# Performance work log

Hardware: AMD Instinct MI355X
Metric: run time of the kernel (lower is better)

## Reference

```python
import jax, jax.numpy as jnp
import numpy as np

LOG_2PI = float(np.log(2.0 * np.pi))


def setup_inputs() -> dict:
    key = jax.random.key(0)
    k1, k2, k3, k4 = jax.random.split(key, 4)
    B, Tin, Tout, D = 32, 512, 2048, 256
    memory = jax.random.normal(k1, (B, Tin, D), dtype=jnp.float32)
    # durations in [1, 7) frames per token (mean ~4 -> ~Tout total frames)
    duration = jax.random.uniform(k2, (B, Tin), dtype=jnp.float32) * 6.0 + 1.0
    # positive Gaussian widths in [0.5, 2.0)
    sigma = jax.random.uniform(k3, (B, Tin), dtype=jnp.float32) * 1.5 + 0.5
    output_lengths = jnp.full((B,), Tout, dtype=jnp.int32)
    mask = jax.random.uniform(k4, (B, Tin)) < 0.1
    return {"memory": memory, "duration": duration, "sigma": sigma,
            "output_lengths": output_lengths, "mask": mask}


def reference(memory, duration, sigma, output_lengths, mask):
    # memory: (B,Tin,D); duration,sigma,mask: (B,Tin); output_lengths: (B,)
    Tout = int(np.max(np.asarray(output_lengths)))
    frames = jnp.arange(Tout, dtype=jnp.float32)[None, None, :]          # (1,1,Tout)
    center = jnp.cumsum(duration, axis=-1) - 0.5 * duration              # (B,Tin)
    c = center[..., None]                                                # (B,Tin,1)
    s = sigma[..., None]                                                 # (B,Tin,1)
    # Normal(loc=c, scale=s).log_prob(frames).exp()
    z = (frames - c) / s
    alignment = jnp.exp(-0.5 * z * z - jnp.log(s) - 0.5 * LOG_2PI)       # (B,Tin,Tout)
    alignment = jnp.where(mask[..., None], 0.0, alignment)               # masked_fill
    attn_weights = alignment / (jnp.sum(alignment, axis=1, keepdims=True) + 1e-8)
    # bmm(attn^T, memory): (B,Tout,Tin) @ (B,Tin,D) -> (B,Tout,D)
    upsampled = jnp.einsum('bit,bid->btd', attn_weights, memory)
    return upsampled, attn_weights
```

## Files before the change

### kernel.cpp

```cpp
#include <hip/hip_runtime.h>
#include <hip/hip_bf16.h>
#include <math.h>

#define HALF_LOG_2PI 0.9189385332046727f
#define WIN 32.0f
#define TILE_T 16

typedef float f32x4 __attribute__((ext_vector_type(4)));

__global__ void prep_k(const float* __restrict__ duration,
                       const float* __restrict__ sigma,
                       const void* __restrict__ mask,
                       float* __restrict__ center,
                       float* __restrict__ amp,
                       float* __restrict__ inv_sigma,
                       int B, int Tin) {
    __shared__ float s[1024];
    __shared__ int s_not[2];
    int b = blockIdx.x, i = threadIdx.x;
    if (i < 2) s_not[i] = 0;
    __syncthreads();
    {
        const unsigned int* mw = (const unsigned int*)mask;
        int nwords = (B * Tin) >> 2;
        int nI = 0, nF = 0;
        for (int k = i; k < nwords; k += blockDim.x) {
            unsigned int w = mw[k];
            nI |= (w != 0u && w != 1u);
            nF |= (w != 0u && w != 0x3F800000u);
        }
        if (nI) atomicOr(&s_not[0], 1);
        if (nF) atomicOr(&s_not[1], 1);
    }
    size_t gi = (size_t)b * Tin + i;
    float d = duration[gi];
    s[i] = d;
    __syncthreads();
    for (int off = 1; off < Tin; off <<= 1) {
        float v = (i >= off) ? s[i - off] : 0.0f;
        __syncthreads();
        s[i] += v;
        __syncthreads();
    }
    float c = s[i] - 0.5f * d;
    int mode = s_not[0] ? (s_not[1] ? 2 : 1) : 0;
    bool m;
    if (mode == 0)      m = ((const int*)mask)[gi] != 0;
    else if (mode == 1) m = ((const float*)mask)[gi] != 0.0f;
    else                m = ((const unsigned char*)mask)[gi] != 0;
    float sg = sigma[gi];
    center[gi]    = c;
    inv_sigma[gi] = 1.0f / sg;
    amp[gi]       = m ? 0.0f : __expf(-__logf(sg) - HALF_LOG_2PI);
}

__global__ __launch_bounds__(256) void denom_k(
        const float* __restrict__ center, const float* __restrict__ amp,
        const float* __restrict__ inv_sigma,
        float* __restrict__ inv_den, int* __restrict__ lo_out,
        int* __restrict__ cnt_out, int Tin, int Tout) {
    __shared__ float sc[1024], sa[1024], si[1024];
    int b = blockIdx.y;
    int t = blockIdx.x * 256 + threadIdx.x;
    for (int i = threadIdx.x; i < Tin; i += 256) {
        size_t g = (size_t)b * Tin + i;
        sc[i] = center[g]; sa[i] = amp[g]; si[i] = inv_sigma[g];
    }
    __syncthreads();
    if (t >= Tout) return;
    float tf = (float)t;
    int lo = 0, hi = Tin;
    while (lo < hi) {
        int mid = (lo + hi) >> 1;
        if (sc[mid] < tf - WIN) lo = mid + 1; else hi = mid;
    }
    float sum = 0.0f;
    int i = lo;
    for (; i < Tin; ++i) {
        float cc = sc[i];
        if (cc > tf + WIN) break;
        float z = (tf - cc) * si[i];
        sum += sa[i] * __expf(-0.5f * z * z);
    }
    size_t g = (size_t)b * Tout + t;
    inv_den[g]  = 1.0f / (sum + 1e-8f);
    lo_out[g]   = lo;
    cnt_out[g]  = i - lo;
}

__global__ __launch_bounds__(256) void attn_k(
        const float* __restrict__ center, const float* __restrict__ amp,
        const float* __restrict__ inv_sigma, const float* __restrict__ inv_den,
        float* __restrict__ attn, int Tin, int Tout) {
    int bi = blockIdx.x;
    int b  = bi / Tin;
    float c = center[bi], a = amp[bi], inv = inv_sigma[bi];
    const float* iden = inv_den + (size_t)b * Tout;
    float* row = attn + (size_t)bi * Tout;
    for (int t4 = threadIdx.x * 4; t4 < Tout; t4 += 256 * 4) {
        f32x4 rv;
        if ((float)(t4 + 3) < c - WIN || (float)t4 > c + WIN) {
            rv = (f32x4)0.0f;
        } else {
            #pragma unroll
            for (int j = 0; j < 4; ++j) {
                float dlt = (float)(t4 + j) - c;
                if (fabsf(dlt) < WIN) {
                    float z = dlt * inv;
                    rv[j] = a * __expf(-0.5f * z * z) * iden[t4 + j];
                } else rv[j] = 0.0f;
            }
        }
        __builtin_nontemporal_store(rv, (f32x4*)(row + t4));
    }
}

__global__ __launch_bounds__(256) void upsample_k(
        const float* __restrict__ mem, const float* __restrict__ center,
        const float* __restrict__ amp, const float* __restrict__ inv_sigma,
        const float* __restrict__ inv_den, const int* __restrict__ lo_ws,
        const int* __restrict__ cnt_ws, float* __restrict__ out,
        int Tin, int Tout, int D) {
    __shared__ __align__(16) float w_s[TILE_T][128];
    __shared__ float s_iden[TILE_T];
    __shared__ int s_lo, s_cnt;
    int nwg = gridDim.x;
    int wid = blockIdx.x;
    int work = wid;
    if ((nwg & 7) == 0) {
        int chunk = nwg >> 3;
        work = (wid & 7) * chunk + (wid >> 3);
    }
    int tpb = Tout / TILE_T;
    int b   = work / tpb;
    int t0  = (work - b * tpb) * TILE_T;
    int tid = threadIdx.x;
    if (tid == 0) {
        size_t g0 = (size_t)b * Tout + t0;
        size_t g1 = g0 + (TILE_T - 1);
        int lo0 = lo_ws[g0];
        int cnt = lo_ws[g1] + cnt_ws[g1] - lo0;
        s_lo  = lo0;
        s_cnt = cnt > 128 ? 128 : cnt;
    }
    if (tid < TILE_T) s_iden[tid] = inv_den[(size_t)b * Tout + t0 + tid];
    __syncthreads();
    int lo0 = s_lo, wcnt = s_cnt;
    #pragma unroll
    for (int rep = 0; rep < (TILE_T * 128) / 256; ++rep) {
        int id = tid + rep * 256;
        int f = id >> 7, w = id & 127;
        float wgt = 0.0f;
        int i = lo0 + w;
        if (w < wcnt && i < Tin) {
            size_t gi = (size_t)b * Tin + i;
            float dlt = (float)(t0 + f) - center[gi];
            if (fabsf(dlt) < WIN) {
                float z = dlt * inv_sigma[gi];
                wgt = amp[gi] * __expf(-0.5f * z * z) * s_iden[f];
            }
        }
        w_s[f][w] = wgt;
    }
    __syncthreads();
    for (int d = tid; d < D; d += 256) {
        float acc[TILE_T];
        #pragma unroll
        for (int f = 0; f < TILE_T; ++f) acc[f] = 0.0f;
        const float* mrow = mem + ((size_t)b * Tin + lo0) * D + d;
        int w4 = wcnt & ~3;
        for (int w = 0; w < w4; w += 4) {
            float m0 = mrow[(size_t)(w + 0) * D];
            float m1 = mrow[(size_t)(w + 1) * D];
            float m2 = mrow[(size_t)(w + 2) * D];
            float m3 = mrow[(size_t)(w + 3) * D];
            #pragma unroll
            for (int f = 0; f < TILE_T; ++f) {
                f32x4 wv = *(const f32x4*)&w_s[f][w];
                acc[f] += wv.x * m0 + wv.y * m1 + wv.z * m2 + wv.w * m3;
            }
        }
        for (int w = w4; w < wcnt; ++w) {
            float m0 = mrow[(size_t)w * D];
            #pragma unroll
            for (int f = 0; f < TILE_T; ++f) acc[f] += w_s[f][w] * m0;
        }
        float* orow = out + ((size_t)b * Tout + t0) * D + d;
        #pragma unroll
        for (int f = 0; f < TILE_T; ++f)
            __builtin_nontemporal_store(acc[f], orow + (size_t)f * D);
    }
}

extern "C" void kernel_launch(void* const* d_in, const int* in_sizes, int n_in,
                              void* d_out, int out_size, void* d_ws, size_t ws_size,
                              hipStream_t stream) {
    const float* memory   = (const float*)d_in[0];
    const float* duration = (const float*)d_in[1];
    const float* sigma    = (const float*)d_in[2];
    const void*  mask     = d_in[4];

    int B    = in_sizes[3];
    int Tin  = in_sizes[1] / B;
    int D    = in_sizes[0] / (B * Tin);
    int Tout = out_size / (B * (D + Tin));

    float* out_up   = (float*)d_out;
    float* out_attn = out_up + (size_t)B * Tout * D;

    float* center = (float*)d_ws;
    float* amp    = center + (size_t)B * Tin;
    float* inv    = amp    + (size_t)B * Tin;
    float* iden   = inv    + (size_t)B * Tin;
    int*   lo     = (int*)(iden + (size_t)B * Tout);
    int*   cnt    = lo + (size_t)B * Tout;

    prep_k<<<B, Tin, 0, stream>>>(duration, sigma, mask,
                                  center, amp, inv, B, Tin);
    denom_k<<<dim3((Tout + 255) / 256, B), 256, 0, stream>>>(
        center, amp, inv, iden, lo, cnt, Tin, Tout);
    attn_k<<<B * Tin, 256, 0, stream>>>(center, amp, inv, iden,
                                        out_attn, Tin, Tout);
    upsample_k<<<(B * Tout) / TILE_T, 256, 0, stream>>>(
        memory, center, amp, inv, iden, lo, cnt, out_up, Tin, Tout, D);
}
```

Before: 62.69 us.

## Fuse denominator, attention and upsample kernels into one interleaved launch

Removes the separate denominator kernel and merges attention-row writing and upsampling into a single launch whose blocks are interleaved two attention rows to one upsample tile. Each block stages center/amp/inv_sigma for its batch in shared memory and recomputes the normalising denominators locally: attention blocks compute them for the window of frames they cover, upsample blocks derive them from the weight tile they already built. This drops two launches and the workspace round-trip for inv_den/lo/cnt, and runs the write-bound attention output alongside the compute-bound upsample. In exchange, denominators are computed redundantly, the upsample tile shrinks to 8 frames so memory rows are reused less, and 12KB of shared memory per block may reduce occupancy.

Measured after the change: 76.51 us. +22.0%, slower.

```diff
diff --git a/kernel.cpp b/kernel.cpp
--- a/kernel.cpp
+++ b/kernel.cpp
@@ -4,7 +4,7 @@
 
 #define HALF_LOG_2PI 0.9189385332046727f
 #define WIN 32.0f
-#define TILE_T 16
+#define TILE_T 8
 
 typedef float f32x4 __attribute__((ext_vector_type(4)));
 
@@ -54,113 +54,119 @@
     amp[gi]       = m ? 0.0f : __expf(-__logf(sg) - HALF_LOG_2PI);
 }
 
-__global__ __launch_bounds__(256) void denom_k(
-        const float* __restrict__ center, const float* __restrict__ amp,
-        const float* __restrict__ inv_sigma,
-        float* __restrict__ inv_den, int* __restrict__ lo_out,
-        int* __restrict__ cnt_out, int Tin, int Tout) {
-    __shared__ float sc[1024], sa[1024], si[1024];
-    int b = blockIdx.y;
-    int t = blockIdx.x * 256 + threadIdx.x;
-    for (int i = threadIdx.x; i < Tin; i += 256) {
-        size_t g = (size_t)b * Tin + i;
-        sc[i] = center[g]; sa[i] = amp[g]; si[i] = inv_sigma[g];
-    }
-    __syncthreads();
-    if (t >= Tout) return;
-    float tf = (float)t;
-    int lo = 0, hi = Tin;
-    while (lo < hi) {
-        int mid = (lo + hi) >> 1;
-        if (sc[mid] < tf - WIN) lo = mid + 1; else hi = mid;
-    }
-    float sum = 0.0f;
-    int i = lo;
-    for (; i < Tin; ++i) {
-        float cc = sc[i];
-        if (cc > tf + WIN) break;
-        float z = (tf - cc) * si[i];
-        sum += sa[i] * __expf(-0.5f * z * z);
-    }
-    size_t g = (size_t)b * Tout + t;
-    inv_den[g]  = 1.0f / (sum + 1e-8f);
-    lo_out[g]   = lo;
-    cnt_out[g]  = i - lo;
-}
-
-__global__ __launch_bounds__(256) void attn_k(
-        const float* __restrict__ center, const float* __restrict__ amp,
-        const float* __restrict__ inv_sigma, const float* __restrict__ inv_den,
-        float* __restrict__ attn, int Tin, int Tout) {
-    int bi = blockIdx.x;
-    int b  = bi / Tin;
-    float c = center[bi], a = amp[bi], inv = inv_sigma[bi];
-    const float* iden = inv_den + (size_t)b * Tout;
-    float* row = attn + (size_t)bi * Tout;
-    for (int t4 = threadIdx.x * 4; t4 < Tout; t4 += 256 * 4) {
-        f32x4 rv;
-        if ((float)(t4 + 3) < c - WIN || (float)t4 > c + WIN) {
-            rv = (f32x4)0.0f;
-        } else {
-            #pragma unroll
-            for (int j = 0; j < 4; ++j) {
-                float dlt = (float)(t4 + j) - c;
-                if (fabsf(dlt) < WIN) {
-                    float z = dlt * inv;
-                    rv[j] = a * __expf(-0.5f * z * z) * iden[t4 + j];
-                } else rv[j] = 0.0f;
-            }
-        }
-        __builtin_nontemporal_store(rv, (f32x4*)(row + t4));
-    }
-}
-
-__global__ __launch_bounds__(256) void upsample_k(
+__global__ __launch_bounds__(256) void fused_k(
         const float* __restrict__ mem, const float* __restrict__ center,
         const float* __restrict__ amp, const float* __restrict__ inv_sigma,
-        const float* __restrict__ inv_den, const int* __restrict__ lo_ws,
-        const int* __restrict__ cnt_ws, float* __restrict__ out,
-        int Tin, int Tout, int D) {
+        float* __restrict__ attn, float* __restrict__ out,
+        int nAttn, int nUp, int Tin, int Tout, int D) {
+    __shared__ __align__(16) float sc[1024], sa[1024], si[1024];
     __shared__ __align__(16) float w_s[TILE_T][128];
-    __shared__ float s_iden[TILE_T];
-    __shared__ int s_lo, s_cnt;
-    int nwg = gridDim.x;
+    __shared__ float s_iden[80];
+
+    int nwg = nAttn + nUp;
     int wid = blockIdx.x;
     int work = wid;
     if ((nwg & 7) == 0) {
         int chunk = nwg >> 3;
         work = (wid & 7) * chunk + (wid >> 3);
     }
+    int aid = -1, uid = -1;
+    if (nAttn == 2 * nUp) {
+        int q = work / 3, r = work - q * 3;
+        if (r == 2) uid = q; else aid = q * 2 + r;
+    } else {
+        if (work < nAttn) aid = work; else uid = work - nAttn;
+    }
+
+    int tid = threadIdx.x;
     int tpb = Tout / TILE_T;
-    int b   = work / tpb;
-    int t0  = (work - b * tpb) * TILE_T;
-    int tid = threadIdx.x;
-    if (tid == 0) {
-        size_t g0 = (size_t)b * Tout + t0;
-        size_t g1 = g0 + (TILE_T - 1);
-        int lo0 = lo_ws[g0];
-        int cnt = lo_ws[g1] + cnt_ws[g1] - lo0;
-        s_lo  = lo0;
-        s_cnt = cnt > 128 ? 128 : cnt;
-    }
-    if (tid < TILE_T) s_iden[tid] = inv_den[(size_t)b * Tout + t0 + tid];
-    __syncthreads();
-    int lo0 = s_lo, wcnt = s_cnt;
+    int b = (aid >= 0) ? (aid / Tin) : (uid / tpb);
+
+    for (int i = tid; i < Tin; i += 256) {
+        size_t g = (size_t)b * Tin + i;
+        sc[i] = center[g]; sa[i] = amp[g]; si[i] = inv_sigma[g];
+    }
+    __syncthreads();
+
+    if (aid >= 0) {
+        int i = aid - b * Tin;
+        float c = sc[i], a = sa[i], inv = si[i];
+        int tlo = max(0, (int)ceilf(c - WIN));
+        int thi = min(Tout - 1, (int)floorf(c + WIN));
+        int nf  = thi - tlo + 1;
+        if (tid < nf) {
+            float tf = (float)(tlo + tid);
+            int lo = 0, hi = Tin;
+            while (lo < hi) {
+                int mid = (lo + hi) >> 1;
+                if (sc[mid] < tf - WIN) lo = mid + 1; else hi = mid;
+            }
+            float sum = 0.0f;
+            for (int j = lo; j < Tin; ++j) {
+                float cc = sc[j];
+                if (cc > tf + WIN) break;
+                float z = (tf - cc) * si[j];
+                sum += sa[j] * __expf(-0.5f * z * z);
+            }
+            s_iden[tid] = 1.0f / (sum + 1e-8f);
+        }
+        __syncthreads();
+        float* row = attn + (size_t)aid * Tout;
+        for (int t4 = tid * 4; t4 < Tout; t4 += 256 * 4) {
+            f32x4 rv;
+            if (t4 + 3 < tlo || t4 > thi) {
+                rv = (f32x4)0.0f;
+            } else {
+                #pragma unroll
+                for (int j = 0; j < 4; ++j) {
+                    int t = t4 + j;
+                    if (t >= tlo && t <= thi) {
+                        float z = ((float)t - c) * inv;
+                        rv[j] = a * __expf(-0.5f * z * z) * s_iden[t - tlo];
+                    } else rv[j] = 0.0f;
+                }
+            }
+            __builtin_nontemporal_store(rv, (f32x4*)(row + t4));
+        }
+        return;
+    }
+
+    int t0 = (uid - b * tpb) * TILE_T;
+    float tfl = (float)t0 - WIN;
+    float tfh = (float)(t0 + TILE_T - 1) + WIN;
+    int lo0 = 0;
+    {   int hi = Tin;
+        while (lo0 < hi) { int mid = (lo0 + hi) >> 1;
+                           if (sc[mid] < tfl) lo0 = mid + 1; else hi = mid; } }
+    int hi1 = lo0;
+    {   int hh = Tin;
+        while (hi1 < hh) { int mid = (hi1 + hh) >> 1;
+                           if (sc[mid] <= tfh) hi1 = mid + 1; else hh = mid; } }
+    int wcnt = hi1 - lo0;
+    if (wcnt > 128) wcnt = 128;
     #pragma unroll
     for (int rep = 0; rep < (TILE_T * 128) / 256; ++rep) {
         int id = tid + rep * 256;
         int f = id >> 7, w = id & 127;
         float wgt = 0.0f;
         int i = lo0 + w;
-        if (w < wcnt && i < Tin) {
-            size_t gi = (size_t)b * Tin + i;
-            float dlt = (float)(t0 + f) - center[gi];
+        if (w < wcnt) {
+            float dlt = (float)(t0 + f) - sc[i];
             if (fabsf(dlt) < WIN) {
-                float z = dlt * inv_sigma[gi];
-                wgt = amp[gi] * __expf(-0.5f * z * z) * s_iden[f];
+                float z = dlt * si[i];
+                wgt = sa[i] * __expf(-0.5f * z * z);
             }
         }
         w_s[f][w] = wgt;
+    }
+    __syncthreads();
+    {
+        int f = tid >> 5, lane = tid & 31;
+        float p = w_s[f][lane] + w_s[f][lane + 32]
+                + w_s[f][lane + 64] + w_s[f][lane + 96];
+        #pragma unroll
+        for (int m = 16; m >= 1; m >>= 1) p += __shfl_xor(p, m, 64);
+        if (lane == 0) s_iden[f] = 1.0f / (p + 1e-8f);
     }
     __syncthreads();
     for (int d = tid; d < D; d += 256) {
@@ -188,7 +194,8 @@
         float* orow = out + ((size_t)b * Tout + t0) * D + d;
         #pragma unroll
         for (int f = 0; f < TILE_T; ++f)
-            __builtin_nontemporal_store(acc[f], orow + (size_t)f * D);
+            __builtin_nontemporal_store(acc[f] * s_iden[f],
+                                        orow + (size_t)f * D);
     }
 }
 
@@ -211,16 +218,12 @@
     float* center = (float*)d_ws;
     float* amp    = center + (size_t)B * Tin;
     float* inv    = amp    + (size_t)B * Tin;
-    float* iden   = inv    + (size_t)B * Tin;
-    int*   lo     = (int*)(iden + (size_t)B * Tout);
-    int*   cnt    = lo + (size_t)B * Tout;
 
     prep_k<<<B, Tin, 0, stream>>>(duration, sigma, mask,
                                   center, amp, inv, B, Tin);
-    denom_k<<<dim3((Tout + 255) / 256, B), 256, 0, stream>>>(
-        center, amp, inv, iden, lo, cnt, Tin, Tout);
-    attn_k<<<B * Tin, 256, 0, stream>>>(center, amp, inv, iden,
-                                        out_attn, Tin, Tout);
-    upsample_k<<<(B * Tout) / TILE_T, 256, 0, stream>>>(
-        memory, center, amp, inv, iden, lo, cnt, out_up, Tin, Tout, D);
+    int nAttn = B * Tin;
+    int nUp   = (B * Tout) / TILE_T;
+    fused_k<<<nAttn + nUp, 256, 0, stream>>>(
+        memory, center, amp, inv, out_attn, out_up,
+        nAttn, nUp, Tin, Tout, D);
 }
```

## Merge attention-write and upsample kernels into one interleaved launch

Applied to the files above, without the earlier changes.

Replaces the separate attention-row writer and upsample kernels with one kernel whose blocks alternate between the two roles by the parity of the work index. Each attention block now writes four rows instead of one. The aim is to overlap the bandwidth-heavy attention stores with the upsample compute and memory reads, and to save one kernel launch. The role mapping assumes equal counts of attention and upsample blocks (B*Tin/4 == B*Tout/16). That holds here, but with other shapes some work would be dropped or indices would run past the end.

Result: no change. 63.81 us (+1.8%).

```diff
diff --git a/kernel.cpp b/kernel.cpp
--- a/kernel.cpp
+++ b/kernel.cpp
@@ -88,39 +88,12 @@
     cnt_out[g]  = i - lo;
 }
 
-__global__ __launch_bounds__(256) void attn_k(
-        const float* __restrict__ center, const float* __restrict__ amp,
-        const float* __restrict__ inv_sigma, const float* __restrict__ inv_den,
-        float* __restrict__ attn, int Tin, int Tout) {
-    int bi = blockIdx.x;
-    int b  = bi / Tin;
-    float c = center[bi], a = amp[bi], inv = inv_sigma[bi];
-    const float* iden = inv_den + (size_t)b * Tout;
-    float* row = attn + (size_t)bi * Tout;
-    for (int t4 = threadIdx.x * 4; t4 < Tout; t4 += 256 * 4) {
-        f32x4 rv;
-        if ((float)(t4 + 3) < c - WIN || (float)t4 > c + WIN) {
-            rv = (f32x4)0.0f;
-        } else {
-            #pragma unroll
-            for (int j = 0; j < 4; ++j) {
-                float dlt = (float)(t4 + j) - c;
-                if (fabsf(dlt) < WIN) {
-                    float z = dlt * inv;
-                    rv[j] = a * __expf(-0.5f * z * z) * iden[t4 + j];
-                } else rv[j] = 0.0f;
-            }
-        }
-        __builtin_nontemporal_store(rv, (f32x4*)(row + t4));
-    }
-}
-
-__global__ __launch_bounds__(256) void upsample_k(
+__global__ __launch_bounds__(256) void attn_up_k(
         const float* __restrict__ mem, const float* __restrict__ center,
         const float* __restrict__ amp, const float* __restrict__ inv_sigma,
         const float* __restrict__ inv_den, const int* __restrict__ lo_ws,
-        const int* __restrict__ cnt_ws, float* __restrict__ out,
-        int Tin, int Tout, int D) {
+        const int* __restrict__ cnt_ws, float* __restrict__ attn,
+        float* __restrict__ out, int Tin, int Tout, int D) {
     __shared__ __align__(16) float w_s[TILE_T][128];
     __shared__ float s_iden[TILE_T];
     __shared__ int s_lo, s_cnt;
@@ -131,10 +104,42 @@
         int chunk = nwg >> 3;
         work = (wid & 7) * chunk + (wid >> 3);
     }
+    int r = work & 1, q = work >> 1;
+    int tid = threadIdx.x;
+
+    if (r == 0) {
+        int rpb = Tin >> 2;
+        int b   = q / rpb;
+        int i0  = (q - b * rpb) * 4;
+        const float* iden = inv_den + (size_t)b * Tout;
+        #pragma unroll
+        for (int rr = 0; rr < 4; ++rr) {
+            int bi = b * Tin + i0 + rr;
+            float c = center[bi], a = amp[bi], inv = inv_sigma[bi];
+            float* row = attn + (size_t)bi * Tout;
+            for (int t4 = tid * 4; t4 < Tout; t4 += 256 * 4) {
+                f32x4 rv;
+                if ((float)(t4 + 3) < c - WIN || (float)t4 > c + WIN) {
+                    rv = (f32x4)0.0f;
+                } else {
+                    #pragma unroll
+                    for (int j = 0; j < 4; ++j) {
+                        float dlt = (float)(t4 + j) - c;
+                        if (fabsf(dlt) < WIN) {
+                            float z = dlt * inv;
+                            rv[j] = a * __expf(-0.5f * z * z) * iden[t4 + j];
+                        } else rv[j] = 0.0f;
+                    }
+                }
+                __builtin_nontemporal_store(rv, (f32x4*)(row + t4));
+            }
+        }
+        return;
+    }
+
     int tpb = Tout / TILE_T;
-    int b   = work / tpb;
-    int t0  = (work - b * tpb) * TILE_T;
-    int tid = threadIdx.x;
+    int b   = q / tpb;
+    int t0  = (q - b * tpb) * TILE_T;
     if (tid == 0) {
         size_t g0 = (size_t)b * Tout + t0;
         size_t g1 = g0 + (TILE_T - 1);
@@ -219,8 +224,9 @@
                                   center, amp, inv, B, Tin);
     denom_k<<<dim3((Tout + 255) / 256, B), 256, 0, stream>>>(
         center, amp, inv, iden, lo, cnt, Tin, Tout);
-    attn_k<<<B * Tin, 256, 0, stream>>>(center, amp, inv, iden,
-                                        out_attn, Tin, Tout);
-    upsample_k<<<(B * Tout) / TILE_T, 256, 0, stream>>>(
-        memory, center, amp, inv, iden, lo, cnt, out_up, Tin, Tout, D);
-}
+    int nAttnQ = (B * Tin) / 4;
+    int nUp    = (B * Tout) / TILE_T;
+    attn_up_k<<<nAttnQ + nUp, 256, 0, stream>>>(
+        memory, center, amp, inv, iden, lo, cnt,
+        out_attn, out_up, Tin, Tout, D);
+}
```

## Fuse prep into denominator kernel and batch four attention rows per block

Applied to the files above, without the earlier changes.

The separate prep kernel is merged into the denominator kernel. Each block recomputes the per-batch cumulative sum with a per-thread chunk plus wavefront shuffle scan, and only the first block in x writes center/amp/inv_sigma to global memory. This removes one kernel launch and the global round-trip for those arrays. The attention kernel now handles four rows per block, cutting the grid size by four to reduce block scheduling overhead. In exchange, the prefix scan and mask-format scan are repeated in every denom block, and the scan assumes Tin is a multiple of 256 and at most 2048.

Result: slower. 65.35 us (+4.2%).

```diff
diff --git a/kernel.cpp b/kernel.cpp
--- a/kernel.cpp
+++ b/kernel.cpp
@@ -8,23 +8,24 @@
 
 typedef float f32x4 __attribute__((ext_vector_type(4)));
 
-__global__ void prep_k(const float* __restrict__ duration,
-                       const float* __restrict__ sigma,
-                       const void* __restrict__ mask,
-                       float* __restrict__ center,
-                       float* __restrict__ amp,
-                       float* __restrict__ inv_sigma,
-                       int B, int Tin) {
-    __shared__ float s[1024];
+__global__ __launch_bounds__(256) void denom_prep_k(
+        const float* __restrict__ duration, const float* __restrict__ sigma,
+        const void* __restrict__ mask,
+        float* __restrict__ center, float* __restrict__ amp,
+        float* __restrict__ inv_sigma, float* __restrict__ inv_den,
+        int* __restrict__ lo_out, int* __restrict__ cnt_out,
+        int B, int Tin, int Tout) {
+    __shared__ float sc[1024], sa[1024], si[1024];
+    __shared__ float s_wsum[4];
     __shared__ int s_not[2];
-    int b = blockIdx.x, i = threadIdx.x;
-    if (i < 2) s_not[i] = 0;
+    int b = blockIdx.y, tid = threadIdx.x;
+    if (tid < 2) s_not[tid] = 0;
     __syncthreads();
     {
         const unsigned int* mw = (const unsigned int*)mask;
         int nwords = (B * Tin) >> 2;
         int nI = 0, nF = 0;
-        for (int k = i; k < nwords; k += blockDim.x) {
+        for (int k = tid; k < nwords; k += 256) {
             unsigned int w = mw[k];
             nI |= (w != 0u && w != 1u);
             nF |= (w != 0u && w != 0x3F800000u);
@@ -32,41 +33,42 @@
         if (nI) atomicOr(&s_not[0], 1);
         if (nF) atomicOr(&s_not[1], 1);
     }
-    size_t gi = (size_t)b * Tin + i;
-    float d = duration[gi];
-    s[i] = d;
-    __syncthreads();
-    for (int off = 1; off < Tin; off <<= 1) {
-        float v = (i >= off) ? s[i - off] : 0.0f;
-        __syncthreads();
-        s[i] += v;
-        __syncthreads();
-    }
-    float c = s[i] - 0.5f * d;
+    int E = Tin >> 8;
+    int base = tid * E;
+    float x[8];
+    float tsum = 0.0f;
+    const float* drow = duration + (size_t)b * Tin;
+    for (int e = 0; e < E; ++e) { x[e] = drow[base + e]; tsum += x[e]; }
+    float isc = tsum;
+    int lane = tid & 63, wv = tid >> 6;
+    #pragma unroll
+    for (int d = 1; d < 64; d <<= 1) {
+        float v = __shfl_up(isc, d, 64);
+        if (lane >= d) isc += v;
+    }
+    if (lane == 63) s_wsum[wv] = isc;
+    __syncthreads();
+    float excl = isc - tsum;
+    for (int w2 = 0; w2 < wv; ++w2) excl += s_wsum[w2];
     int mode = s_not[0] ? (s_not[1] ? 2 : 1) : 0;
-    bool m;
-    if (mode == 0)      m = ((const int*)mask)[gi] != 0;
-    else if (mode == 1) m = ((const float*)mask)[gi] != 0.0f;
-    else                m = ((const unsigned char*)mask)[gi] != 0;
-    float sg = sigma[gi];
-    center[gi]    = c;
-    inv_sigma[gi] = 1.0f / sg;
-    amp[gi]       = m ? 0.0f : __expf(-__logf(sg) - HALF_LOG_2PI);
-}
-
-__global__ __launch_bounds__(256) void denom_k(
-        const float* __restrict__ center, const float* __restrict__ amp,
-        const float* __restrict__ inv_sigma,
-        float* __restrict__ inv_den, int* __restrict__ lo_out,
-        int* __restrict__ cnt_out, int Tin, int Tout) {
-    __shared__ float sc[1024], sa[1024], si[1024];
-    int b = blockIdx.y;
-    int t = blockIdx.x * 256 + threadIdx.x;
-    for (int i = threadIdx.x; i < Tin; i += 256) {
-        size_t g = (size_t)b * Tin + i;
-        sc[i] = center[g]; sa[i] = amp[g]; si[i] = inv_sigma[g];
-    }
-    __syncthreads();
+    float run = excl;
+    for (int e = 0; e < E; ++e) {
+        float c = run + 0.5f * x[e];
+        run += x[e];
+        int i = base + e;
+        size_t gi = (size_t)b * Tin + i;
+        bool m;
+        if (mode == 0)      m = ((const int*)mask)[gi] != 0;
+        else if (mode == 1) m = ((const float*)mask)[gi] != 0.0f;
+        else                m = ((const unsigned char*)mask)[gi] != 0;
+        float sg = sigma[gi];
+        float a  = m ? 0.0f : __expf(-__logf(sg) - HALF_LOG_2PI);
+        float is = 1.0f / sg;
+        sc[i] = c; sa[i] = a; si[i] = is;
+        if (blockIdx.x == 0) { center[gi] = c; amp[gi] = a; inv_sigma[gi] = is; }
+    }
+    __syncthreads();
+    int t = blockIdx.x * 256 + tid;
     if (t >= Tout) return;
     float tf = (float)t;
     int lo = 0, hi = Tin;
@@ -83,35 +85,42 @@
         sum += sa[i] * __expf(-0.5f * z * z);
     }
     size_t g = (size_t)b * Tout + t;
-    inv_den[g]  = 1.0f / (sum + 1e-8f);
-    lo_out[g]   = lo;
-    cnt_out[g]  = i - lo;
+    inv_den[g] = 1.0f / (sum + 1e-8f);
+    lo_out[g]  = lo;
+    cnt_out[g] = i - lo;
 }
 
 __global__ __launch_bounds__(256) void attn_k(
         const float* __restrict__ center, const float* __restrict__ amp,
         const float* __restrict__ inv_sigma, const float* __restrict__ inv_den,
         float* __restrict__ attn, int Tin, int Tout) {
-    int bi = blockIdx.x;
-    int b  = bi / Tin;
-    float c = center[bi], a = amp[bi], inv = inv_sigma[bi];
+    int q   = blockIdx.x;
+    int rpb = Tin >> 2;
+    int b   = q / rpb;
+    int i0  = (q - b * rpb) * 4;
     const float* iden = inv_den + (size_t)b * Tout;
-    float* row = attn + (size_t)bi * Tout;
-    for (int t4 = threadIdx.x * 4; t4 < Tout; t4 += 256 * 4) {
-        f32x4 rv;
-        if ((float)(t4 + 3) < c - WIN || (float)t4 > c + WIN) {
-            rv = (f32x4)0.0f;
-        } else {
-            #pragma unroll
-            for (int j = 0; j < 4; ++j) {
-                float dlt = (float)(t4 + j) - c;
-                if (fabsf(dlt) < WIN) {
-                    float z = dlt * inv;
-                    rv[j] = a * __expf(-0.5f * z * z) * iden[t4 + j];
-                } else rv[j] = 0.0f;
+    int tid = threadIdx.x;
+    #pragma unroll
+    for (int rr = 0; rr < 4; ++rr) {
+        int bi = b * Tin + i0 + rr;
+        float c = center[bi], a = amp[bi], inv = inv_sigma[bi];
+        float* row = attn + (size_t)bi * Tout;
+        for (int t4 = tid * 4; t4 < Tout; t4 += 256 * 4) {
+            f32x4 rv;
+            if ((float)(t4 + 3) < c - WIN || (float)t4 > c + WIN) {
+                rv = (f32x4)0.0f;
+            } else {
+                #pragma unroll
+                for (int j = 0; j < 4; ++j) {
+                    float dlt = (float)(t4 + j) - c;
+                    if (fabsf(dlt) < WIN) {
+                        float z = dlt * inv;
+                        rv[j] = a * __expf(-0.5f * z * z) * iden[t4 + j];
+                    } else rv[j] = 0.0f;
+                }
             }
-        }
-        __builtin_nontemporal_store(rv, (f32x4*)(row + t4));
+            __builtin_nontemporal_store(rv, (f32x4*)(row + t4));
+        }
     }
 }
 
@@ -215,12 +224,11 @@
     int*   lo     = (int*)(iden + (size_t)B * Tout);
     int*   cnt    = lo + (size_t)B * Tout;
 
-    prep_k<<<B, Tin, 0, stream>>>(duration, sigma, mask,
-                                  center, amp, inv, B, Tin);
-    denom_k<<<dim3((Tout + 255) / 256, B), 256, 0, stream>>>(
-        center, amp, inv, iden, lo, cnt, Tin, Tout);
-    attn_k<<<B * Tin, 256, 0, stream>>>(center, amp, inv, iden,
-                                        out_attn, Tin, Tout);
+    denom_prep_k<<<dim3((Tout + 255) / 256, B), 256, 0, stream>>>(
+        duration, sigma, mask, center, amp, inv, iden, lo, cnt,
+        B, Tin, Tout);
+    attn_k<<<(B * Tin) / 4, 256, 0, stream>>>(center, amp, inv, iden,
+                                              out_attn, Tin, Tout);
     upsample_k<<<(B * Tout) / TILE_T, 256, 0, stream>>>(
         memory, center, amp, inv, iden, lo, cnt, out_up, Tin, Tout, D);
 }
```
